# Performance work log

Hardware: AMD Instinct MI355X
Metric: run time of the kernel (lower is better)

## Reference

```python
import jax, jax.numpy as jnp
import numpy as np

B, T, D = 16, 3000, 512
GROUPS, NUM_VARS = 2, 320
VQ_DIM = 256
VAR_DIM = VQ_DIM // GROUPS  # 128


def setup_inputs() -> dict:
    key = jax.random.key(0)
    k_x, k_w, k_v = jax.random.split(key, 3)
    x = jax.random.normal(k_x, (B, T, D), dtype=jnp.float32)
    # weight_proj: Linear(dim, groups*num_vars), weight ~ N(0,1), bias = 0
    W = jax.random.normal(k_w, (GROUPS * NUM_VARS, D), dtype=jnp.float32)
    b = jnp.zeros((GROUPS * NUM_VARS,), dtype=jnp.float32)
    # codebook: nn.init.uniform_ -> U[0,1); combine_groups=False -> num_groups = GROUPS
    codebook = jax.random.uniform(k_v, (1, GROUPS * NUM_VARS, VAR_DIM), dtype=jnp.float32)
    return {"x": x, "W": W, "b": b, "codebook": codebook}


def reference(x, W, b, codebook):
    """Eval-mode GumbelVectorQuantizer forward (hard argmax path).

    Returns (quantized [B,T,VQ_DIM], avg_probs [GROUPS, NUM_VARS]).
    """
    Bv, Tv, Dv = x.shape
    N = Bv * Tv
    # weight_proj
    logits = jnp.einsum('nd,vd->nv', x.reshape(N, Dv), W) + b  # [N, G*V]
    logits = logits.reshape(N, GROUPS, NUM_VARS)
    # hard one-hot over codebook entries per group
    k = jnp.argmax(logits, axis=-1)                             # [N, G] int
    hard = jax.nn.one_hot(k, NUM_VARS, dtype=logits.dtype)      # [N, G, V]
    # avg probs (softmax in fp32, mean over tokens)
    avg_probs = jax.nn.softmax(logits.astype(jnp.float32), axis=-1).mean(axis=0)  # [G, V]
    # dense multiply-sum against codebook == gather of selected code vectors
    vars_g = codebook.reshape(GROUPS, NUM_VARS, VAR_DIM)        # [G, V, d]
    out = jnp.einsum('ngv,gvd->ngd', hard, vars_g)              # [N, G, d]
    out = out.reshape(Bv, Tv, GROUPS * VAR_DIM)                 # [B, T, VQ_DIM]
    return out, avg_probs
```

## Files before the change

### kernel.cpp

```cpp
#include <hip/hip_runtime.h>

#define GROUPS 2
#define NUM_VARS 320
#define NVT 640
#define DIM 512
#define VAR_DIM 128
#define NTOK 48000
#define TM 32
#define TMF 64
#define BLOCK 256
#define KCH 256
#define XP 264
#define NT16 40
#define NKS 16
#define NTILE (NTOK / 16)
#define TSTRIDE (NKS * 2 * 512)

typedef short bf16x8 __attribute__((ext_vector_type(8)));
typedef float f32x4  __attribute__((ext_vector_type(4)));
typedef unsigned short u16;
typedef u16 u16x4 __attribute__((ext_vector_type(4)));
typedef u16 u16x8 __attribute__((ext_vector_type(8)));

__device__ inline u16 bf16_rne(float f) {
    unsigned u = __builtin_bit_cast(unsigned, f);
    return (u16)((u + 0x7fffu + ((u >> 16) & 1u)) >> 16);
}
__device__ inline void split2(float f, u16& h, u16& l) {
    h = bf16_rne(f);
    float fh = __builtin_bit_cast(float, (unsigned)h << 16);
    l = bf16_rne(f - fh);
}

__device__ __forceinline__ void gll16(const void* g, void* l) {
    __builtin_amdgcn_global_load_lds(
        (const __attribute__((address_space(1))) unsigned int*)g,
        (__attribute__((address_space(3))) unsigned int*)l,
        16, 0, 0);
}

__global__ void pack_w_kernel(const float* __restrict__ W, u16* __restrict__ Wpk) {
    int idx = blockIdx.x * blockDim.x + threadIdx.x;
    if (idx >= NT16 * NKS * 64 * 8) return;
    int j    = idx & 7;
    int lane = (idx >> 3) & 63;
    int ks   = (idx >> 9) & 15;
    int v16  = idx >> 13;
    int row  = v16 * 16 + (lane & 15);
    int k    = ks * 32 + 8 * (lane >> 4) + j;
    u16 h, l;
    split2(W[(size_t)row * DIM + k], h, l);
    size_t base = (size_t)((v16 * NKS + ks) * 2) * 512 + lane * 8 + j;
    Wpk[base]       = h;
    Wpk[base + 512] = l;
}

__global__ void split_x_pack_kernel(const float* __restrict__ x,
                                    u16* __restrict__ xpk) {
    const int gw   = (blockIdx.x * blockDim.x + threadIdx.x) >> 6;
    const int lane = threadIdx.x & 63;
    if (gw >= NTILE) return;
    const int l15 = lane & 15, l4 = lane >> 4;
    const float* xr = x + (size_t)(gw * 16 + l15) * DIM + 8 * l4;
    u16* dst = xpk + (size_t)gw * TSTRIDE + lane * 8;
#pragma unroll 4
    for (int ks = 0; ks < NKS; ++ks) {
        float4 a = *(const float4*)(xr + ks * 32);
        float4 b = *(const float4*)(xr + ks * 32 + 4);
        u16x8 hv, lv; u16 h, l;
        split2(a.x, h, l); hv[0] = h; lv[0] = l;
        split2(a.y, h, l); hv[1] = h; lv[1] = l;
        split2(a.z, h, l); hv[2] = h; lv[2] = l;
        split2(a.w, h, l); hv[3] = h; lv[3] = l;
        split2(b.x, h, l); hv[4] = h; lv[4] = l;
        split2(b.y, h, l); hv[5] = h; lv[5] = l;
        split2(b.z, h, l); hv[6] = h; lv[6] = l;
        split2(b.w, h, l); hv[7] = h; lv[7] = l;
        *(u16x8*)(dst + ks * 1024)       = hv;
        *(u16x8*)(dst + ks * 1024 + 512) = lv;
    }
}

__global__ __launch_bounds__(BLOCK, 2)
void vq_mfma_reg_kernel(const float* __restrict__ x,
                        const float* __restrict__ W,
                        const u16* __restrict__ xpk,
                        const u16* __restrict__ Wpk,
                        const float* __restrict__ bias,
                        const float* __restrict__ codebook,
                        float* __restrict__ out,
                        float* __restrict__ avg_out) {
    __shared__ u16 As[3][4][2][512];
    __shared__ float avg_s[NUM_VARS];
    __shared__ float tv_s[TMF][4][2];
    __shared__ int   ti_s[TMF][4][2];
    __shared__ float m_s[TMF], gap_s[TMF], sum_s[TMF];
    __shared__ int   i1_s[TMF], i2_s[TMF], kb_s[TMF];

    const int tid  = threadIdx.x;
    const int lane = tid & 63;
    const int ty   = tid >> 6;
    const int l15  = lane & 15;
    const int l4   = lane >> 4;
    const int g    = blockIdx.x & 1;
    const int n0   = (blockIdx.x >> 1) * TMF;

    for (int i = tid; i < NUM_VARS; i += BLOCK) avg_s[i] = 0.f;

    const f32x4 zf = {0.f, 0.f, 0.f, 0.f};
    f32x4 acc[4][5];
#pragma unroll
    for (int rt = 0; rt < 4; ++rt)
#pragma unroll
        for (int ct = 0; ct < 5; ++ct) acc[rt][ct] = zf;

    const u16* xa_st = xpk + (size_t)((blockIdx.x >> 1) * 4 + ty) * TSTRIDE + lane * 8;
    const u16* wpk_b = Wpk + (size_t)(g * 20 + ty * 5) * TSTRIDE + lane * 8;

    gll16(xa_st,        &As[0][ty][0][0]);
    gll16(xa_st + 512,  &As[0][ty][1][0]);
    gll16(xa_st + 1024, &As[1][ty][0][0]);
    gll16(xa_st + 1536, &As[1][ty][1][0]);
    asm volatile("s_waitcnt vmcnt(2)" ::: "memory");
    __builtin_amdgcn_s_barrier();

#pragma unroll 1
    for (int ks = 0; ks < NKS; ++ks) {
        const int cur = ks % 3;
        bf16x8 bh[5], bl[5];
#pragma unroll
        for (int ct = 0; ct < 5; ++ct) {
            const u16* wp = wpk_b + (size_t)(ct * NKS + ks) * 1024;
            bh[ct] = *(const bf16x8*)wp;
            bl[ct] = *(const bf16x8*)(wp + 512);
        }
#pragma unroll
        for (int rt = 0; rt < 4; ++rt) {
            bf16x8 ah = *(const bf16x8*)&As[cur][rt][0][lane * 8];
            bf16x8 al = *(const bf16x8*)&As[cur][rt][1][lane * 8];
#pragma unroll
            for (int ct = 0; ct < 5; ++ct) {
                acc[rt][ct] = __builtin_amdgcn_mfma_f32_16x16x32_bf16(ah, bh[ct], acc[rt][ct], 0, 0, 0);
                acc[rt][ct] = __builtin_amdgcn_mfma_f32_16x16x32_bf16(ah, bl[ct], acc[rt][ct], 0, 0, 0);
                acc[rt][ct] = __builtin_amdgcn_mfma_f32_16x16x32_bf16(al, bh[ct], acc[rt][ct], 0, 0, 0);
            }
        }
        if (ks + 2 < NKS) {
            const int nb = (ks + 2) % 3;
            gll16(xa_st + (size_t)(ks + 2) * 1024,       &As[nb][ty][0][0]);
            gll16(xa_st + (size_t)(ks + 2) * 1024 + 512, &As[nb][ty][1][0]);
        }
        if (ks < NKS - 2) {
            asm volatile("s_waitcnt vmcnt(2) lgkmcnt(0)" ::: "memory");
        } else {
            asm volatile("s_waitcnt vmcnt(0) lgkmcnt(0)" ::: "memory");
        }
        __builtin_amdgcn_s_barrier();
    }

#pragma unroll
    for (int ct = 0; ct < 5; ++ct) {
        float bv = bias[g * NUM_VARS + ty * 80 + ct * 16 + l15];
#pragma unroll
        for (int rt = 0; rt < 4; ++rt)
#pragma unroll
            for (int j = 0; j < 4; ++j) acc[rt][ct][j] += bv;
    }

#pragma unroll
    for (int rt = 0; rt < 4; ++rt)
#pragma unroll
    for (int j = 0; j < 4; ++j) {
        float v1 = -3.4e38f, v2 = -3.4e38f;
        int   i1 = 0x7fffffff, i2 = 0x7fffffff;
#pragma unroll
        for (int ct = 0; ct < 5; ++ct) {
            float val = acc[rt][ct][j];
            int   vi  = ty * 80 + ct * 16 + l15;
            if ((val > v1) || (val == v1 && vi < i1)) { v2 = v1; i2 = i1; v1 = val; i1 = vi; }
            else if ((val > v2) || (val == v2 && vi < i2)) { v2 = val; i2 = vi; }
        }
#pragma unroll
        for (int off = 1; off <= 8; off <<= 1) {
            float o1 = __shfl_xor(v1, off); int oi1 = __shfl_xor(i1, off);
            float o2 = __shfl_xor(v2, off); int oi2 = __shfl_xor(i2, off);
            if ((o1 > v1) || (o1 == v1 && oi1 < i1)) { v2 = v1; i2 = i1; v1 = o1; i1 = oi1; }
            else if ((o1 > v2) || (o1 == v2 && oi1 < i2)) { v2 = o1; i2 = oi1; }
            if ((o2 > v1) || (o2 == v1 && oi2 < i1)) { v2 = v1; i2 = i1; v1 = o2; i1 = oi2; }
            else if ((o2 > v2) || (o2 == v2 && oi2 < i2)) { v2 = o2; i2 = oi2; }
        }
        if (l15 == 0) {
            const int T = rt * 16 + l4 * 4 + j;
            tv_s[T][ty][0] = v1; tv_s[T][ty][1] = v2;
            ti_s[T][ty][0] = i1; ti_s[T][ty][1] = i2;
        }
    }
    __syncthreads();

    if (tid < TMF) {
        float v1 = -3.4e38f, v2 = -3.4e38f;
        int   i1 = 0x7fffffff, i2 = 0x7fffffff;
#pragma unroll
        for (int w = 0; w < 4; ++w)
#pragma unroll
            for (int q = 0; q < 2; ++q) {
                float val = tv_s[tid][w][q]; int vi = ti_s[tid][w][q];
                if ((val > v1) || (val == v1 && vi < i1)) { v2 = v1; i2 = i1; v1 = val; i1 = vi; }
                else if ((val > v2) || (val == v2 && vi < i2)) { v2 = val; i2 = vi; }
            }
        m_s[tid] = v1; gap_s[tid] = v1 - v2;
        i1_s[tid] = i1; i2_s[tid] = i2; kb_s[tid] = i1; sum_s[tid] = 0.f;
    }
    __syncthreads();

#pragma unroll
    for (int rt = 0; rt < 4; ++rt)
#pragma unroll
    for (int j = 0; j < 4; ++j) {
        const int T = rt * 16 + l4 * 4 + j;
        const float m = m_s[T];
        float s = 0.f;
#pragma unroll
        for (int ct = 0; ct < 5; ++ct) {
            float e = __expf(acc[rt][ct][j] - m);
            acc[rt][ct][j] = e;
            s += e;
        }
#pragma unroll
        for (int off = 1; off <= 8; off <<= 1) s += __shfl_xor(s, off);
        if (l15 == 0) atomicAdd(&sum_s[T], s);
    }
    __syncthreads();

#pragma unroll
    for (int ct = 0; ct < 5; ++ct) {
        float tot = 0.f;
#pragma unroll
        for (int rt = 0; rt < 4; ++rt)
#pragma unroll
        for (int j = 0; j < 4; ++j) {
            const int T = rt * 16 + l4 * 4 + j;
            float v = acc[rt][ct][j] * (1.f / sum_s[T]);
            v += __shfl_xor(v, 16);
            v += __shfl_xor(v, 32);
            tot += v;
        }
        if (l4 == 0) avg_s[ty * 80 + ct * 16 + l15] += tot;
    }

    for (int t16 = 0; t16 < 16; ++t16) {
        const int T = ty * 16 + t16;
        if (gap_s[T] <= 0.05f) {
            const int i1 = i1_s[T], i2 = i2_s[T];
            const float* xr = x + (size_t)(n0 + T) * DIM;
            const float* w1 = W + (size_t)(g * NUM_VARS + i1) * DIM;
            const float* w2 = W + (size_t)(g * NUM_VARS + i2) * DIM;
            double d1 = 0.0, d2 = 0.0;
            for (int k = lane; k < DIM; k += 64) {
                double xv = (double)xr[k];
                d1 += xv * (double)w1[k];
                d2 += xv * (double)w2[k];
            }
#pragma unroll
            for (int off = 1; off <= 32; off <<= 1) {
                d1 += __shfl_xor(d1, off);
                d2 += __shfl_xor(d2, off);
            }
            d1 += (double)bias[g * NUM_VARS + i1];
            d2 += (double)bias[g * NUM_VARS + i2];
            if (lane == 0)
                kb_s[T] = (d2 > d1 || (d2 == d1 && i2 < i1)) ? i2 : i1;
        }
    }
    __syncthreads();

#pragma unroll
    for (int i = 0; i < 8; ++i) {
        const int f = tid + i * BLOCK;
        const int T = f >> 5, p = f & 31;
        const int kb = kb_s[T];
        float4 cv = *(const float4*)(codebook +
                     (size_t)(g * NUM_VARS + kb) * VAR_DIM + p * 4);
        *(float4*)(out + (size_t)(n0 + T) * (GROUPS * VAR_DIM) + g * VAR_DIM + p * 4) = cv;
    }

    const float scale = 1.f / (float)NTOK;
    for (int i = tid; i < NUM_VARS; i += BLOCK)
        atomicAdd(&avg_out[g * NUM_VARS + i], avg_s[i] * scale);
}

template <bool USE_WQ>
__global__ __launch_bounds__(BLOCK, 2)
void vq_mfma_kernel(const float* __restrict__ x,
                    const float* __restrict__ W,
                    const u16* __restrict__ Wpk,
                    const float* __restrict__ bias,
                    const float* __restrict__ codebook,
                    float* __restrict__ out,
                    float* __restrict__ avg_out) {
    __shared__ u16 xs_hi[TM][XP];
    __shared__ u16 xs_lo[TM][XP];
    __shared__ float avg_s[NUM_VARS];
    __shared__ float tv_s[TM][4][2];
    __shared__ int   ti_s[TM][4][2];
    __shared__ float m_s[TM], gap_s[TM], sum_s[TM];
    __shared__ int   i1_s[TM], i2_s[TM], kb_s[TM];

    const int tid  = threadIdx.x;
    const int lane = tid & 63;
    const int ty   = tid >> 6;
    const int l15  = lane & 15;
    const int l4   = lane >> 4;
    const int g    = blockIdx.x & 1;
    const int n0   = (blockIdx.x >> 1) * TM;

    for (int i = tid; i < NUM_VARS; i += BLOCK) avg_s[i] = 0.f;

    const f32x4 zf = {0.f, 0.f, 0.f, 0.f};
    f32x4 acc[2][5];
#pragma unroll
    for (int rt = 0; rt < 2; ++rt)
#pragma unroll
        for (int ct = 0; ct < 5; ++ct) acc[rt][ct] = zf;

    const int vw = g * NUM_VARS + ty * 80;

    for (int c = 0; c < DIM / KCH; ++c) {
        __syncthreads();
        {
            const int t  = tid >> 3;
            const int kb = (tid & 7) * 4;
            const float* xp = x + (size_t)(n0 + t) * DIM + c * KCH;
#pragma unroll
            for (int i = 0; i < 8; ++i) {
                const int k = kb + i * 32;
                float4 v = *(const float4*)(xp + k);
                u16x4 hv, lv; u16 h, l;
                split2(v.x, h, l); hv[0] = h; lv[0] = l;
                split2(v.y, h, l); hv[1] = h; lv[1] = l;
                split2(v.z, h, l); hv[2] = h; lv[2] = l;
                split2(v.w, h, l); hv[3] = h; lv[3] = l;
                *(u16x4*)&xs_hi[t][k] = hv;
                *(u16x4*)&xs_lo[t][k] = lv;
            }
        }
        __syncthreads();
#pragma unroll
        for (int ks = 0; ks < KCH / 32; ++ks) {
            const int ko = ks * 32 + 8 * l4;
            bf16x8 ah0 = *(const bf16x8*)&xs_hi[l15][ko];
            bf16x8 al0 = *(const bf16x8*)&xs_lo[l15][ko];
            bf16x8 ah1 = *(const bf16x8*)&xs_hi[16 + l15][ko];
            bf16x8 al1 = *(const bf16x8*)&xs_lo[16 + l15][ko];
            const int ksg = c * (KCH / 32) + ks;
#pragma unroll
            for (int ct = 0; ct < 5; ++ct) {
                bf16x8 bh, bl;
                if (USE_WQ) {
                    const int v16g = g * (NUM_VARS / 16) + ty * 5 + ct;
                    const u16* wp = Wpk + (size_t)((v16g * NKS + ksg) * 2) * 512 + lane * 8;
                    bh = *(const bf16x8*)wp;
                    bl = *(const bf16x8*)(wp + 512);
                } else {
                    const int kg = ksg * 32 + 8 * l4;
                    const float* wp = W + (size_t)(vw + ct * 16 + l15) * DIM + kg;
                    float4 wa = *(const float4*)wp;
                    float4 wb = *(const float4*)(wp + 4);
                    u16 h, l;
                    split2(wa.x, h, l); bh[0] = (short)h; bl[0] = (short)l;
                    split2(wa.y, h, l); bh[1] = (short)h; bl[1] = (short)l;
                    split2(wa.z, h, l); bh[2] = (short)h; bl[2] = (short)l;
                    split2(wa.w, h, l); bh[3] = (short)h; bl[3] = (short)l;
                    split2(wb.x, h, l); bh[4] = (short)h; bl[4] = (short)l;
                    split2(wb.y, h, l); bh[5] = (short)h; bl[5] = (short)l;
                    split2(wb.z, h, l); bh[6] = (short)h; bl[6] = (short)l;
                    split2(wb.w, h, l); bh[7] = (short)h; bl[7] = (short)l;
                }
                acc[0][ct] = __builtin_amdgcn_mfma_f32_16x16x32_bf16(ah0, bh, acc[0][ct], 0, 0, 0);
                acc[0][ct] = __builtin_amdgcn_mfma_f32_16x16x32_bf16(ah0, bl, acc[0][ct], 0, 0, 0);
                acc[0][ct] = __builtin_amdgcn_mfma_f32_16x16x32_bf16(al0, bh, acc[0][ct], 0, 0, 0);
                acc[1][ct] = __builtin_amdgcn_mfma_f32_16x16x32_bf16(ah1, bh, acc[1][ct], 0, 0, 0);
                acc[1][ct] = __builtin_amdgcn_mfma_f32_16x16x32_bf16(ah1, bl, acc[1][ct], 0, 0, 0);
                acc[1][ct] = __builtin_amdgcn_mfma_f32_16x16x32_bf16(al1, bh, acc[1][ct], 0, 0, 0);
            }
        }
    }

#pragma unroll
    for (int ct = 0; ct < 5; ++ct) {
        float bv = bias[vw + ct * 16 + l15];
#pragma unroll
        for (int rt = 0; rt < 2; ++rt)
#pragma unroll
            for (int j = 0; j < 4; ++j) acc[rt][ct][j] += bv;
    }

#pragma unroll
    for (int rt = 0; rt < 2; ++rt)
#pragma unroll
    for (int j = 0; j < 4; ++j) {
        float v1 = -3.4e38f, v2 = -3.4e38f;
        int   i1 = 0x7fffffff, i2 = 0x7fffffff;
#pragma unroll
        for (int ct = 0; ct < 5; ++ct) {
            float val = acc[rt][ct][j];
            int   vi  = ty * 80 + ct * 16 + l15;
            if ((val > v1) || (val == v1 && vi < i1)) { v2 = v1; i2 = i1; v1 = val; i1 = vi; }
            else if ((val > v2) || (val == v2 && vi < i2)) { v2 = val; i2 = vi; }
        }
#pragma unroll
        for (int off = 1; off <= 8; off <<= 1) {
            float o1 = __shfl_xor(v1, off); int oi1 = __shfl_xor(i1, off);
            float o2 = __shfl_xor(v2, off); int oi2 = __shfl_xor(i2, off);
            if ((o1 > v1) || (o1 == v1 && oi1 < i1)) { v2 = v1; i2 = i1; v1 = o1; i1 = oi1; }
            else if ((o1 > v2) || (o1 == v2 && oi1 < i2)) { v2 = o1; i2 = oi1; }
            if ((o2 > v1) || (o2 == v1 && oi2 < i1)) { v2 = v1; i2 = i1; v1 = o2; i1 = oi2; }
            else if ((o2 > v2) || (o2 == v2 && oi2 < i2)) { v2 = o2; i2 = oi2; }
        }
        if (l15 == 0) {
            const int T = rt * 16 + l4 * 4 + j;
            tv_s[T][ty][0] = v1; tv_s[T][ty][1] = v2;
            ti_s[T][ty][0] = i1; ti_s[T][ty][1] = i2;
        }
    }
    __syncthreads();

    if (tid < TM) {
        float v1 = -3.4e38f, v2 = -3.4e38f;
        int   i1 = 0x7fffffff, i2 = 0x7fffffff;
#pragma unroll
        for (int w = 0; w < 4; ++w)
#pragma unroll
            for (int q = 0; q < 2; ++q) {
                float val = tv_s[tid][w][q]; int vi = ti_s[tid][w][q];
                if ((val > v1) || (val == v1 && vi < i1)) { v2 = v1; i2 = i1; v1 = val; i1 = vi; }
                else if ((val > v2) || (val == v2 && vi < i2)) { v2 = val; i2 = vi; }
            }
        m_s[tid] = v1; gap_s[tid] = v1 - v2;
        i1_s[tid] = i1; i2_s[tid] = i2; kb_s[tid] = i1; sum_s[tid] = 0.f;
    }
    __syncthreads();

#pragma unroll
    for (int rt = 0; rt < 2; ++rt)
#pragma unroll
    for (int j = 0; j < 4; ++j) {
        const int T = rt * 16 + l4 * 4 + j;
        const float m = m_s[T];
        float s = 0.f;
#pragma unroll
        for (int ct = 0; ct < 5; ++ct) {
            float e = expf(acc[rt][ct][j] - m);
            acc[rt][ct][j] = e;
            s += e;
        }
#pragma unroll
        for (int off = 1; off <= 8; off <<= 1) s += __shfl_xor(s, off);
        if (l15 == 0) atomicAdd(&sum_s[T], s);
    }
    __syncthreads();

#pragma unroll
    for (int ct = 0; ct < 5; ++ct) {
        float tot = 0.f;
#pragma unroll
        for (int rt = 0; rt < 2; ++rt)
#pragma unroll
        for (int j = 0; j < 4; ++j) {
            const int T = rt * 16 + l4 * 4 + j;
            float v = acc[rt][ct][j] / sum_s[T];
            v += __shfl_xor(v, 16);
            v += __shfl_xor(v, 32);
            tot += v;
        }
        if (l4 == 0) avg_s[ty * 80 + ct * 16 + l15] += tot;
    }

    for (int t8 = 0; t8 < 8; ++t8) {
        const int T = ty * 8 + t8;
        if (gap_s[T] <= 0.05f) {
            const int i1 = i1_s[T], i2 = i2_s[T];
            const float* xr = x + (size_t)(n0 + T) * DIM;
            const float* w1 = W + (size_t)(g * NUM_VARS + i1) * DIM;
            const float* w2 = W + (size_t)(g * NUM_VARS + i2) * DIM;
            double d1 = 0.0, d2 = 0.0;
            for (int k = lane; k < DIM; k += 64) {
                double xv = (double)xr[k];
                d1 += xv * (double)w1[k];
                d2 += xv * (double)w2[k];
            }
#pragma unroll
            for (int off = 1; off <= 32; off <<= 1) {
                d1 += __shfl_xor(d1, off);
                d2 += __shfl_xor(d2, off);
            }
            d1 += (double)bias[g * NUM_VARS + i1];
            d2 += (double)bias[g * NUM_VARS + i2];
            if (lane == 0)
                kb_s[T] = (d2 > d1 || (d2 == d1 && i2 < i1)) ? i2 : i1;
        }
    }
    __syncthreads();

#pragma unroll
    for (int i = 0; i < 4; ++i) {
        const int f = tid + i * BLOCK;
        const int T = f >> 5, p = f & 31;
        const int kb = kb_s[T];
        float4 cv = *(const float4*)(codebook +
                     (size_t)(g * NUM_VARS + kb) * VAR_DIM + p * 4);
        *(float4*)(out + (size_t)(n0 + T) * (GROUPS * VAR_DIM) + g * VAR_DIM + p * 4) = cv;
    }

    const float scale = 1.f / (float)NTOK;
    for (int i = tid; i < NUM_VARS; i += BLOCK)
        atomicAdd(&avg_out[g * NUM_VARS + i], avg_s[i] * scale);
}

extern "C" void kernel_launch(void* const* d_in, const int* in_sizes, int n_in,
                              void* d_out, int out_size, void* d_ws, size_t ws_size,
                              hipStream_t stream) {
    const float* x  = (const float*)d_in[0];
    const float* W  = (const float*)d_in[1];
    const float* b  = (const float*)d_in[2];
    const float* cb = (const float*)d_in[3];
    float* out = (float*)d_out;
    float* avg = out + (size_t)NTOK * GROUPS * VAR_DIM;

    hipMemsetAsync(avg, 0, NVT * sizeof(float), stream);

    const size_t wpk_bytes = (size_t)NT16 * NKS * 2 * 512 * sizeof(u16);
    const size_t xpk_bytes = (size_t)NTILE * NKS * 2 * 512 * sizeof(u16);
    const size_t full_bytes = wpk_bytes + xpk_bytes;

    if (ws_size >= full_bytes) {
        u16* Wpk = (u16*)d_ws;
        u16* xpk = (u16*)((char*)d_ws + wpk_bytes);
        pack_w_kernel<<<(NT16 * NKS * 64 * 8 + 255) / 256, 256, 0, stream>>>(W, Wpk);
        split_x_pack_kernel<<<(NTILE + 3) / 4, 256, 0, stream>>>(x, xpk);
        vq_mfma_reg_kernel<<<(NTOK / TMF) * GROUPS, BLOCK, 0, stream>>>(
            x, W, xpk, Wpk, b, cb, out, avg);
    } else if (ws_size >= wpk_bytes) {
        u16* Wpk = (u16*)d_ws;
        pack_w_kernel<<<(NT16 * NKS * 64 * 8 + 255) / 256, 256, 0, stream>>>(W, Wpk);
        vq_mfma_kernel<true><<<(NTOK / TM) * GROUPS, BLOCK, 0, stream>>>(x, W, Wpk, b, cb, out, avg);
    } else {
        vq_mfma_kernel<false><<<(NTOK / TM) * GROUPS, BLOCK, 0, stream>>>(x, W, nullptr, b, cb, out, avg);
    }
}
```

Baseline: 187.0 us.

## Fuse x bf16 hi/lo split into the MFMA GEMM kernel, drop pre-pack pass

Result: faster. 164.5 us (-12.0%).

```diff
diff --git a/kernel.cpp b/kernel.cpp
--- a/kernel.cpp
+++ b/kernel.cpp
@@ -13,7 +13,6 @@
 #define XP 264
 #define NT16 40
 #define NKS 16
-#define NTILE (NTOK / 16)
 #define TSTRIDE (NKS * 2 * 512)
 
 typedef short bf16x8 __attribute__((ext_vector_type(8)));
@@ -31,12 +30,16 @@
     float fh = __builtin_bit_cast(float, (unsigned)h << 16);
     l = bf16_rne(f - fh);
 }
-
-__device__ __forceinline__ void gll16(const void* g, void* l) {
-    __builtin_amdgcn_global_load_lds(
-        (const __attribute__((address_space(1))) unsigned int*)g,
-        (__attribute__((address_space(3))) unsigned int*)l,
-        16, 0, 0);
+__device__ inline void split8(float4 a, float4 b, u16x8& hv, u16x8& lv) {
+    u16 h, l;
+    split2(a.x, h, l); hv[0] = h; lv[0] = l;
+    split2(a.y, h, l); hv[1] = h; lv[1] = l;
+    split2(a.z, h, l); hv[2] = h; lv[2] = l;
+    split2(a.w, h, l); hv[3] = h; lv[3] = l;
+    split2(b.x, h, l); hv[4] = h; lv[4] = l;
+    split2(b.y, h, l); hv[5] = h; lv[5] = l;
+    split2(b.z, h, l); hv[6] = h; lv[6] = l;
+    split2(b.w, h, l); hv[7] = h; lv[7] = l;
 }
 
 __global__ void pack_w_kernel(const float* __restrict__ W, u16* __restrict__ Wpk) {
@@ -55,41 +58,14 @@
     Wpk[base + 512] = l;
 }
 
-__global__ void split_x_pack_kernel(const float* __restrict__ x,
-                                    u16* __restrict__ xpk) {
-    const int gw   = (blockIdx.x * blockDim.x + threadIdx.x) >> 6;
-    const int lane = threadIdx.x & 63;
-    if (gw >= NTILE) return;
-    const int l15 = lane & 15, l4 = lane >> 4;
-    const float* xr = x + (size_t)(gw * 16 + l15) * DIM + 8 * l4;
-    u16* dst = xpk + (size_t)gw * TSTRIDE + lane * 8;
-#pragma unroll 4
-    for (int ks = 0; ks < NKS; ++ks) {
-        float4 a = *(const float4*)(xr + ks * 32);
-        float4 b = *(const float4*)(xr + ks * 32 + 4);
-        u16x8 hv, lv; u16 h, l;
-        split2(a.x, h, l); hv[0] = h; lv[0] = l;
-        split2(a.y, h, l); hv[1] = h; lv[1] = l;
-        split2(a.z, h, l); hv[2] = h; lv[2] = l;
-        split2(a.w, h, l); hv[3] = h; lv[3] = l;
-        split2(b.x, h, l); hv[4] = h; lv[4] = l;
-        split2(b.y, h, l); hv[5] = h; lv[5] = l;
-        split2(b.z, h, l); hv[6] = h; lv[6] = l;
-        split2(b.w, h, l); hv[7] = h; lv[7] = l;
-        *(u16x8*)(dst + ks * 1024)       = hv;
-        *(u16x8*)(dst + ks * 1024 + 512) = lv;
-    }
-}
-
 __global__ __launch_bounds__(BLOCK, 2)
-void vq_mfma_reg_kernel(const float* __restrict__ x,
-                        const float* __restrict__ W,
-                        const u16* __restrict__ xpk,
-                        const u16* __restrict__ Wpk,
-                        const float* __restrict__ bias,
-                        const float* __restrict__ codebook,
-                        float* __restrict__ out,
-                        float* __restrict__ avg_out) {
+void vq_mfma_fused_kernel(const float* __restrict__ x,
+                          const float* __restrict__ W,
+                          const u16* __restrict__ Wpk,
+                          const float* __restrict__ bias,
+                          const float* __restrict__ codebook,
+                          float* __restrict__ out,
+                          float* __restrict__ avg_out) {
     __shared__ u16 As[3][4][2][512];
     __shared__ float avg_s[NUM_VARS];
     __shared__ float tv_s[TMF][4][2];
@@ -114,15 +90,19 @@
 #pragma unroll
         for (int ct = 0; ct < 5; ++ct) acc[rt][ct] = zf;
 
-    const u16* xa_st = xpk + (size_t)((blockIdx.x >> 1) * 4 + ty) * TSTRIDE + lane * 8;
+    const float* xsrc = x + (size_t)(n0 + ty * 16 + l15) * DIM + 8 * l4;
     const u16* wpk_b = Wpk + (size_t)(g * 20 + ty * 5) * TSTRIDE + lane * 8;
 
-    gll16(xa_st,        &As[0][ty][0][0]);
-    gll16(xa_st + 512,  &As[0][ty][1][0]);
-    gll16(xa_st + 1024, &As[1][ty][0][0]);
-    gll16(xa_st + 1536, &As[1][ty][1][0]);
-    asm volatile("s_waitcnt vmcnt(2)" ::: "memory");
-    __builtin_amdgcn_s_barrier();
+#pragma unroll
+    for (int s = 0; s < 2; ++s) {
+        float4 a = *(const float4*)(xsrc + s * 32);
+        float4 b = *(const float4*)(xsrc + s * 32 + 4);
+        u16x8 hv, lv;
+        split8(a, b, hv, lv);
+        *(u16x8*)&As[s][ty][0][lane * 8] = hv;
+        *(u16x8*)&As[s][ty][1][lane * 8] = lv;
+    }
+    __syncthreads();
 
 #pragma unroll 1
     for (int ks = 0; ks < NKS; ++ks) {
@@ -134,6 +114,12 @@
             bh[ct] = *(const bf16x8*)wp;
             bl[ct] = *(const bf16x8*)(wp + 512);
         }
+        float4 sx0, sx1;
+        const int kst = ks + 2;
+        if (kst < NKS) {
+            sx0 = *(const float4*)(xsrc + (size_t)kst * 32);
+            sx1 = *(const float4*)(xsrc + (size_t)kst * 32 + 4);
+        }
 #pragma unroll
         for (int rt = 0; rt < 4; ++rt) {
             bf16x8 ah = *(const bf16x8*)&As[cur][rt][0][lane * 8];
@@ -145,16 +131,15 @@
                 acc[rt][ct] = __builtin_amdgcn_mfma_f32_16x16x32_bf16(al, bh[ct], acc[rt][ct], 0, 0, 0);
             }
         }
-        if (ks + 2 < NKS) {
-            const int nb = (ks + 2) % 3;
-            gll16(xa_st + (size_t)(ks + 2) * 1024,       &As[nb][ty][0][0]);
-            gll16(xa_st + (size_t)(ks + 2) * 1024 + 512, &As[nb][ty][1][0]);
-        }
-        if (ks < NKS - 2) {
-            asm volatile("s_waitcnt vmcnt(2) lgkmcnt(0)" ::: "memory");
-        } else {
-            asm volatile("s_waitcnt vmcnt(0) lgkmcnt(0)" ::: "memory");
-        }
+        if (kst < NKS) {
+            const int nb = kst % 3;
+            u16x8 hv, lv;
+            split8(sx0, sx1, hv, lv);
+            *(u16x8*)&As[nb][ty][0][lane * 8] = hv;
+            *(u16x8*)&As[nb][ty][1][lane * 8] = lv;
+        }
+        asm volatile("s_waitcnt lgkmcnt(0)" ::: "memory");
+        __builtin_amdgcn_sched_barrier(0);
         __builtin_amdgcn_s_barrier();
     }
 
@@ -530,20 +515,12 @@
     hipMemsetAsync(avg, 0, NVT * sizeof(float), stream);
 
     const size_t wpk_bytes = (size_t)NT16 * NKS * 2 * 512 * sizeof(u16);
-    const size_t xpk_bytes = (size_t)NTILE * NKS * 2 * 512 * sizeof(u16);
-    const size_t full_bytes = wpk_bytes + xpk_bytes;
-
-    if (ws_size >= full_bytes) {
-        u16* Wpk = (u16*)d_ws;
-        u16* xpk = (u16*)((char*)d_ws + wpk_bytes);
-        pack_w_kernel<<<(NT16 * NKS * 64 * 8 + 255) / 256, 256, 0, stream>>>(W, Wpk);
-        split_x_pack_kernel<<<(NTILE + 3) / 4, 256, 0, stream>>>(x, xpk);
-        vq_mfma_reg_kernel<<<(NTOK / TMF) * GROUPS, BLOCK, 0, stream>>>(
-            x, W, xpk, Wpk, b, cb, out, avg);
-    } else if (ws_size >= wpk_bytes) {
+
+    if (ws_size >= wpk_bytes) {
         u16* Wpk = (u16*)d_ws;
         pack_w_kernel<<<(NT16 * NKS * 64 * 8 + 255) / 256, 256, 0, stream>>>(W, Wpk);
-        vq_mfma_kernel<true><<<(NTOK / TM) * GROUPS, BLOCK, 0, stream>>>(x, W, Wpk, b, cb, out, avg);
+        vq_mfma_fused_kernel<<<(NTOK / TMF) * GROUPS, BLOCK, 0, stream>>>(
+            x, W, Wpk, b, cb, out, avg);
     } else {
         vq_mfma_kernel<false><<<(NTOK / TM) * GROUPS, BLOCK, 0, stream>>>(x, W, nullptr, b, cb, out, avg);
     }
```
